# Performance work log

Measured on AMD Instinct MI355X. Metric: run time of the kernel, lower is better.

Reference implementation:

```python
import jax, jax.numpy as jnp
import numpy as np

NUM_HEADS = 16
EPS = 1e-6

def _rmsnorm(h, w):
    h32 = h.astype(jnp.float32)
    var = jnp.mean(h32 * h32, axis=-1, keepdims=True)
    return (w * (h32 * jax.lax.rsqrt(var + EPS))).astype(h.dtype)

def setup_inputs() -> dict:
    key = jax.random.key(0)
    ks = jax.random.split(key, 4)
    B, N, C = 16, 1024, 1024
    x = jax.random.normal(ks[0], (B, N, C), dtype=jnp.float32)
    qkv_w = jax.random.normal(ks[1], (3 * C, C), dtype=jnp.float32) * (C ** -0.5)
    proj_w = jax.random.normal(ks[2], (C, C), dtype=jnp.float32) * (C ** -0.5)
    proj_b = jnp.zeros((C,), dtype=jnp.float32)
    q_norm_w = jnp.ones((C // NUM_HEADS,), dtype=jnp.float32)
    k_norm_w = jnp.ones((C // NUM_HEADS,), dtype=jnp.float32)
    return {"x": x, "qkv_w": qkv_w, "proj_w": proj_w, "proj_b": proj_b,
            "q_norm_w": q_norm_w, "k_norm_w": k_norm_w}

def reference(x, qkv_w, proj_w, proj_b, q_norm_w, k_norm_w):
    B, N, C = x.shape
    H = NUM_HEADS
    Dh = C // H
    scale = Dh ** -0.5  # qk_scale default; temperature = 1.0
    # QKV projection (no bias): [B,N,3,H,Dh]
    qkv = (x @ qkv_w.T).reshape(B, N, 3, H, Dh)
    q, k, v = qkv[:, :, 0], qkv[:, :, 1], qkv[:, :, 2]
    # per-head QK RMSNorm (fp32 internally)
    q = _rmsnorm(q, q_norm_w)
    k = _rmsnorm(k, k_norm_w)
    # explicit softmax attention: [B,H,N,N]
    attn = jnp.einsum('bnhd,bmhd->bhnm', q * scale, k)
    attn = jax.nn.softmax(attn, axis=-1)
    out = jnp.einsum('bhnm,bmhd->bnhd', attn, v).reshape(B, N, C)
    return out @ proj_w.T + proj_b
```

## Files before the change

### kernel.cpp

```cpp
#include <hip/hip_runtime.h>
#include <hip/hip_bf16.h>

typedef __attribute__((ext_vector_type(8))) __bf16 bf16x8;
typedef __attribute__((ext_vector_type(4))) __bf16 bf16x4;
typedef __attribute__((ext_vector_type(4))) float f32x4;

#define AS1(p) ((__attribute__((address_space(1))) void*)(p))
#define AS3(p) ((__attribute__((address_space(3))) void*)(p))

__global__ void f2b_kernel(const float4* __restrict__ in, bf16x4* __restrict__ out, int n4) {
    int idx = blockIdx.x * blockDim.x + threadIdx.x;
    int stride = gridDim.x * blockDim.x;
    for (int i = idx; i < n4; i += stride) {
        float4 v = in[i];
        bf16x4 o;
        o[0] = (__bf16)v.x; o[1] = (__bf16)v.y; o[2] = (__bf16)v.z; o[3] = (__bf16)v.w;
        out[i] = o;
    }
}

template<int MODE>
__global__ __launch_bounds__(512, 2)
void gemm256(const __bf16* __restrict__ A, const __bf16* __restrict__ Bw,
             const float* __restrict__ bias, const float* __restrict__ qw,
             const float* __restrict__ kw, float* __restrict__ Cf,
             __bf16* __restrict__ Cb, __bf16* __restrict__ Vt,
             int M, int K, int nbn, int ldc)
{
    __shared__ __bf16 Asl[4][256 * 32];
    __shared__ __bf16 Bsl[4][256 * 32];
    const int tid = threadIdx.x, l = tid & 63, w = tid >> 6;
    const int fr = l & 15, fk = l >> 4;

    const int cpx = gridDim.x >> 3;
    const int wg = (blockIdx.x & 7) * cpx + (blockIdx.x >> 3);
    const int bm = wg / nbn, bn = wg % nbn;

    const __bf16* Ag = A + (size_t)bm * 256 * K;
    const __bf16* Bg = Bw + (size_t)bn * 256 * K;

    const int arow = tid >> 2;
    const int uch = (tid & 3) ^ ((arow >> 1) & 3);
    const size_t ga = (size_t)arow * K + uch * 8;
    const size_t ga2 = ga + (size_t)128 * K;

    const int axc = (fk ^ ((fr >> 1) & 3)) * 16;
    int aoff[8], boff[4];
    #pragma unroll
    for (int m = 0; m < 8; ++m)
        aoff[m] = ((w >> 2) * 128 + m * 16 + fr) * 64 + axc;
    #pragma unroll
    for (int n = 0; n < 4; ++n)
        boff[n] = ((w & 3) * 64 + n * 16 + fr) * 64 + axc;

    f32x4 acc[8][4] = {};

#define STAGE256(S) do {                                                                    \
    const int sb_ = (S) & 3;                                                                \
    __builtin_amdgcn_global_load_lds(AS1(Ag + (size_t)(S) * 32 + ga),                       \
        AS3((char*)&Asl[sb_][0] + tid * 16), 16, 0, 0);                                     \
    __builtin_amdgcn_global_load_lds(AS1(Ag + (size_t)(S) * 32 + ga2),                      \
        AS3((char*)&Asl[sb_][0] + tid * 16 + 8192), 16, 0, 0);                              \
    __builtin_amdgcn_global_load_lds(AS1(Bg + (size_t)(S) * 32 + ga),                       \
        AS3((char*)&Bsl[sb_][0] + tid * 16), 16, 0, 0);                                     \
    __builtin_amdgcn_global_load_lds(AS1(Bg + (size_t)(S) * 32 + ga2),                      \
        AS3((char*)&Bsl[sb_][0] + tid * 16 + 8192), 16, 0, 0);                              \
} while (0)

#define PHASE256(S, VMSTR, DOSTAGE) do {                                                    \
    asm volatile("s_waitcnt vmcnt(" VMSTR ")" ::: "memory");                                \
    __builtin_amdgcn_s_barrier();                                                           \
    __builtin_amdgcn_sched_barrier(0);                                                      \
    const int pb_ = (S) & 3;                                                                \
    bf16x8 af[8], bfv[4];                                                                   \
    _Pragma("unroll")                                                                       \
    for (int m = 0; m < 8; ++m)                                                             \
        af[m] = *(const bf16x8*)((const char*)&Asl[pb_][0] + aoff[m]);                      \
    _Pragma("unroll")                                                                       \
    for (int n = 0; n < 4; ++n)                                                             \
        bfv[n] = *(const bf16x8*)((const char*)&Bsl[pb_][0] + boff[n]);                     \
    if (DOSTAGE) STAGE256((S) + 3);                                                         \
    __builtin_amdgcn_s_setprio(1);                                                          \
    _Pragma("unroll")                                                                       \
    for (int m = 0; m < 8; ++m)                                                             \
        _Pragma("unroll")                                                                   \
        for (int n = 0; n < 4; ++n)                                                         \
            acc[m][n] = __builtin_amdgcn_mfma_f32_16x16x32_bf16(af[m], bfv[n], acc[m][n], 0, 0, 0); \
    __builtin_amdgcn_s_setprio(0);                                                          \
} while (0)

    const int S = K >> 5;
    STAGE256(0); STAGE256(1); STAGE256(2);
    for (int s = 0; s < S - 2; ++s)
        PHASE256(s, "8", (s + 3 < S));
    PHASE256(S - 2, "4", false);
    PHASE256(S - 1, "0", false);
#undef PHASE256
#undef STAGE256

    const int rb0 = bm * 256 + (w >> 2) * 128 + fk * 4;
    const int cb0 = bn * 256 + (w & 3) * 64;

    if (MODE == 1) {
        #pragma unroll
        for (int m = 0; m < 8; ++m)
            #pragma unroll
            for (int n = 0; n < 4; ++n) {
                const int col = cb0 + n * 16 + fr;
                const float bv = bias[col];
                #pragma unroll
                for (int r = 0; r < 4; ++r)
                    Cf[(size_t)(rb0 + m * 16 + r) * ldc + col] = acc[m][n][r] + bv;
            }
    } else {
        const int sect = bn >> 2;
        if (sect < 2) {
            const float* wp = (sect == 0) ? qw : kw;
            float wn[4];
            #pragma unroll
            for (int n = 0; n < 4; ++n) wn[n] = wp[((w & 3) * 64 + n * 16 + fr) & 63];
            #pragma unroll
            for (int m = 0; m < 8; ++m) {
                float sc[4];
                #pragma unroll
                for (int r = 0; r < 4; ++r) {
                    float ps = 0.f;
                    #pragma unroll
                    for (int n = 0; n < 4; ++n) ps += acc[m][n][r] * acc[m][n][r];
                    ps += __shfl_xor(ps, 1); ps += __shfl_xor(ps, 2);
                    ps += __shfl_xor(ps, 4); ps += __shfl_xor(ps, 8);
                    sc[r] = rsqrtf(ps * (1.0f / 64.0f) + 1e-6f);
                    if (sect == 0) sc[r] *= 0.18033688011112042f;
                }
                #pragma unroll
                for (int n = 0; n < 4; ++n)
                    #pragma unroll
                    for (int r = 0; r < 4; ++r)
                        Cb[(size_t)(rb0 + m * 16 + r) * ldc + cb0 + n * 16 + fr] =
                            (__bf16)(acc[m][n][r] * sc[r] * wn[n]);
            }
        } else {
            #pragma unroll
            for (int m = 0; m < 8; ++m) {
                const int tok = rb0 + m * 16;
                const int b = tok >> 10, ntok = tok & 1023;
                #pragma unroll
                for (int n = 0; n < 4; ++n) {
                    const int vd = (bn - 8) * 256 + (w & 3) * 64 + n * 16 + fr;
                    bf16x4 pk;
                    #pragma unroll
                    for (int r = 0; r < 4; ++r) pk[r] = (__bf16)acc[m][n][r];
                    *(bf16x4*)&Vt[((size_t)((b * 16 + (vd >> 6)) * 64 + (vd & 63))) * 1024 + ntok] = pk;
                }
            }
        }
    }
}

__global__ __launch_bounds__(256, 2)
void attn_kernel(const __bf16* __restrict__ qkv, const __bf16* __restrict__ vt,
                 __bf16* __restrict__ ao)
{
    __shared__ __bf16 Ks[4][64 * 64];
    __shared__ __bf16 Vs[4][64 * 64];
    __shared__ __bf16 Pl[4][2 * 16 * 64];
    const int tid = threadIdx.x, l = tid & 63, w = tid >> 6;
    const int fr = l & 15, fk = l >> 4;
    const int sw = (fr & 7) << 4;

    const int bi = blockIdx.x;
    const int L = (bi & 7) * 128 + (bi >> 3);
    const int qb = L & 3, h = (L >> 2) & 15, b = L >> 6;

    const __bf16* Kg = qkv + (size_t)b * 1024 * 2048 + 1024 + h * 64;
    const __bf16* Vg = vt + (size_t)((b * 16 + h) * 64) * 1024;
    const int srow = tid >> 3, scp = tid & 7;

    const int c8 = (scp ^ (srow & 7)) * 8;
    const size_t kO0 = (size_t)srow * 2048 + c8, kO1 = kO0 + 32 * 2048;
    const size_t vO0 = (size_t)srow * 1024 + c8, vO1 = vO0 + 32 * 1024;
    char* ksd = (char*)&Ks[0][0] + tid * 16;
    char* vsd = (char*)&Vs[0][0] + tid * 16;

#define STAGE(KT) do {                                                                    \
    char* dk_ = ksd + ((KT) & 3) * 8192;                                                  \
    char* dv_ = vsd + ((KT) & 3) * 8192;                                                  \
    __builtin_amdgcn_global_load_lds(AS1(Kg + (size_t)(KT) * 131072 + kO0), AS3(dk_), 16, 0, 0); \
    __builtin_amdgcn_global_load_lds(AS1(Kg + (size_t)(KT) * 131072 + kO1), AS3(dk_ + 4096), 16, 0, 0); \
    __builtin_amdgcn_global_load_lds(AS1(Vg + (KT) * 64 + vO0), AS3(dv_), 16, 0, 0);      \
    __builtin_amdgcn_global_load_lds(AS1(Vg + (KT) * 64 + vO1), AS3(dv_ + 4096), 16, 0, 0); \
} while (0)

    STAGE(0); STAGE(1);

    const int qrow0 = b * 1024 + qb * 256 + w * 64;
    bf16x8 qf[4][2];
    #pragma unroll
    for (int qi = 0; qi < 4; ++qi)
        #pragma unroll
        for (int dc = 0; dc < 2; ++dc)
            qf[qi][dc] = *(const bf16x8*)&qkv[(size_t)(qrow0 + qi * 16 + fr) * 2048
                                              + h * 64 + dc * 32 + fk * 8];

    const int kb0 = fr * 128 + ((fk ^ (fr & 7)) * 16);
    const int kb1 = fr * 128 + (((4 + fk) ^ (fr & 7)) * 16);
    const char* KsB = (const char*)&Ks[0][0];
    const char* VsB = (const char*)&Vs[0][0];

    char* Pw = (char*)&Pl[w][0];
    const int pw0 = (fr * 128 + 0 * 32 + fk * 8) ^ sw;
    const int pw1 = (fr * 128 + 1 * 32 + fk * 8) ^ sw;
    const int pw2 = (fr * 128 + 2 * 32 + fk * 8) ^ sw;
    const int pw3 = (fr * 128 + 3 * 32 + fk * 8) ^ sw;
    const int pr0 = (fr * 128 + 0 * 64 + fk * 16) ^ sw;
    const int pr1 = (fr * 128 + 1 * 64 + fk * 16) ^ sw;

    bf16x8 onesf;
    #pragma unroll
    for (int i = 0; i < 8; ++i) onesf[i] = (__bf16)1.0f;

    f32x4 oacc[4][4] = {};
    f32x4 lacc[4] = {};

    for (int p = 0; p < 8; ++p) {
        asm volatile("s_waitcnt vmcnt(0)" ::: "memory");
        __builtin_amdgcn_s_barrier();
        __builtin_amdgcn_sched_barrier(0);
        if (p < 7) { STAGE(2 * p + 2); STAGE(2 * p + 3); }

        #pragma unroll
        for (int kh = 0; kh < 2; ++kh) {
            const int cb = (((p & 1) << 1) | kh) * 8192;
            bf16x8 kf[4][2], vf[4][2];
            #pragma unroll
            for (int n = 0; n < 4; ++n) {
                kf[n][0] = *(const bf16x8*)(KsB + cb + kb0 + n * 2048);
                kf[n][1] = *(const bf16x8*)(KsB + cb + kb1 + n * 2048);
            }
            #pragma unroll
            for (int nd = 0; nd < 4; ++nd) {
                vf[nd][0] = *(const bf16x8*)(VsB + cb + kb0 + nd * 2048);
                vf[nd][1] = *(const bf16x8*)(VsB + cb + kb1 + nd * 2048);
            }

            #pragma unroll
            for (int qi = 0; qi < 4; ++qi) {
                const int pq = (qi & 1) * 2048;
                f32x4 sacc[4] = {};
                #pragma unroll
                for (int n = 0; n < 4; ++n)
                    #pragma unroll
                    for (int dc = 0; dc < 2; ++dc)
                        sacc[n] = __builtin_amdgcn_mfma_f32_16x16x32_bf16(kf[n][dc], qf[qi][dc],
                                                                          sacc[n], 0, 0, 0);

                #pragma unroll
                for (int n = 0; n < 4; ++n) {
                    bf16x4 pk;
                    #pragma unroll
                    for (int r = 0; r < 4; ++r)
                        pk[r] = (__bf16)__builtin_amdgcn_exp2f(sacc[n][r]);
                    const int pwn = (n == 0) ? pw0 : (n == 1) ? pw1 : (n == 2) ? pw2 : pw3;
                    *(bf16x4*)(Pw + pq + pwn) = pk;
                }

                bf16x8 pf0 = *(const bf16x8*)(Pw + pq + pr0);
                bf16x8 pf1 = *(const bf16x8*)(Pw + pq + pr1);
                lacc[qi] = __builtin_amdgcn_mfma_f32_16x16x32_bf16(pf0, onesf, lacc[qi], 0, 0, 0);
                lacc[qi] = __builtin_amdgcn_mfma_f32_16x16x32_bf16(pf1, onesf, lacc[qi], 0, 0, 0);
                #pragma unroll
                for (int nd = 0; nd < 4; ++nd) {
                    oacc[qi][nd] = __builtin_amdgcn_mfma_f32_16x16x32_bf16(pf0, vf[nd][0],
                                                                           oacc[qi][nd], 0, 0, 0);
                    oacc[qi][nd] = __builtin_amdgcn_mfma_f32_16x16x32_bf16(pf1, vf[nd][1],
                                                                           oacc[qi][nd], 0, 0, 0);
                }
            }
        }
    }

    #pragma unroll
    for (int qi = 0; qi < 4; ++qi) {
        float inv[4];
        #pragma unroll
        for (int r = 0; r < 4; ++r)
            inv[r] = __builtin_amdgcn_rcpf(lacc[qi][r]);
        #pragma unroll
        for (int nd = 0; nd < 4; ++nd)
            #pragma unroll
            for (int r = 0; r < 4; ++r)
                ao[(size_t)(qrow0 + qi * 16 + fk * 4 + r) * 1024 + h * 64 + nd * 16 + fr] =
                    (__bf16)(oacc[qi][nd][r] * inv[r]);
    }
#undef STAGE
}

extern "C" void kernel_launch(void* const* d_in, const int* in_sizes, int n_in,
                              void* d_out, int out_size, void* d_ws, size_t ws_size,
                              hipStream_t stream)
{
    const float* x      = (const float*)d_in[0];
    const float* qkv_w  = (const float*)d_in[1];
    const float* proj_w = (const float*)d_in[2];
    const float* proj_b = (const float*)d_in[3];
    const float* qnw    = (const float*)d_in[4];
    const float* knw    = (const float*)d_in[5];

    char* ws = (char*)d_ws;
    __bf16* xb    = (__bf16*)(ws);
    __bf16* wqkv  = (__bf16*)(ws + 33554432);
    __bf16* wproj = (__bf16*)(ws + 39845888);
    __bf16* qkv   = (__bf16*)(ws + 41943040);
    __bf16* vt    = (__bf16*)(ws + 109051904);
    __bf16* ao    = (__bf16*)(ws + 142606336);

    f2b_kernel<<<2048, 256, 0, stream>>>((const float4*)x,      (bf16x4*)xb,    16777216 / 4);
    f2b_kernel<<<2048, 256, 0, stream>>>((const float4*)qkv_w,  (bf16x4*)wqkv,  3145728 / 4);
    f2b_kernel<<<1024, 256, 0, stream>>>((const float4*)proj_w, (bf16x4*)wproj, 1048576 / 4);

    gemm256<0><<<768, 512, 0, stream>>>(xb, wqkv, nullptr, qnw, knw,
                                        nullptr, qkv, vt, 16384, 1024, 12, 2048);
    attn_kernel<<<1024, 256, 0, stream>>>(qkv, vt, ao);
    gemm256<1><<<256, 512, 0, stream>>>(ao, wproj, proj_b, nullptr, nullptr,
                                        (float*)d_out, nullptr, nullptr, 16384, 1024, 4, 1024);
}
```

Before: 255.6 us.

## Software-pipeline QK and PV MFMAs in attention; merge weight cast kernels

The attention inner loop is restructured so the QK^T MFMAs and exp for the next query tile are issued while the PV and row-sum MFMAs for the current tile run, using the double-buffered per-wave P scratch. K fragments are now loaded inside the QK step and V fragments are reloaded at the half-point. This hides the latency of exp and the LDS round-trip for P behind matrix work, at the cost of more live registers. Separately, the two weight fp32-to-bf16 casts are merged into one launch to save a kernel launch.

```diff
diff --git a/kernel.cpp b/kernel.cpp
--- a/kernel.cpp
+++ b/kernel.cpp
@@ -16,6 +16,18 @@
         bf16x4 o;
         o[0] = (__bf16)v.x; o[1] = (__bf16)v.y; o[2] = (__bf16)v.z; o[3] = (__bf16)v.w;
         out[i] = o;
+    }
+}
+
+__global__ void f2b2_kernel(const float4* __restrict__ a, bf16x4* __restrict__ oa, int na4,
+                            const float4* __restrict__ b, bf16x4* __restrict__ ob, int nb4) {
+    int idx = blockIdx.x * blockDim.x + threadIdx.x;
+    int stride = gridDim.x * blockDim.x;
+    for (int i = idx; i < na4 + nb4; i += stride) {
+        const float4 v = (i < na4) ? a[i] : b[i - na4];
+        bf16x4 o;
+        o[0] = (__bf16)v.x; o[1] = (__bf16)v.y; o[2] = (__bf16)v.z; o[3] = (__bf16)v.w;
+        if (i < na4) oa[i] = o; else ob[i - na4] = o;
     }
 }
 
@@ -222,60 +234,80 @@
     f32x4 oacc[4][4] = {};
     f32x4 lacc[4] = {};
 
+#define QK8(SA, QI, CB) do {                                                              \
+    _Pragma("unroll")                                                                     \
+    for (int n_ = 0; n_ < 4; ++n_) {                                                      \
+        bf16x8 k0_ = *(const bf16x8*)(KsB + (CB) + kb0 + n_ * 2048);                      \
+        bf16x8 k1_ = *(const bf16x8*)(KsB + (CB) + kb1 + n_ * 2048);                      \
+        SA[n_] = __builtin_amdgcn_mfma_f32_16x16x32_bf16(k0_, qf[QI][0], SA[n_], 0, 0, 0);\
+        SA[n_] = __builtin_amdgcn_mfma_f32_16x16x32_bf16(k1_, qf[QI][1], SA[n_], 0, 0, 0);\
+    } } while (0)
+
+#define EXPW(SA, PQ) do {                                                                 \
+    _Pragma("unroll")                                                                     \
+    for (int n_ = 0; n_ < 4; ++n_) {                                                      \
+        bf16x4 pk_;                                                                       \
+        _Pragma("unroll")                                                                 \
+        for (int r_ = 0; r_ < 4; ++r_)                                                    \
+            pk_[r_] = (__bf16)__builtin_amdgcn_exp2f(SA[n_][r_]);                         \
+        const int pwn_ = (n_ == 0) ? pw0 : (n_ == 1) ? pw1 : (n_ == 2) ? pw2 : pw3;       \
+        *(bf16x4*)(Pw + (PQ) + pwn_) = pk_;                                               \
+    } } while (0)
+
     for (int p = 0; p < 8; ++p) {
         asm volatile("s_waitcnt vmcnt(0)" ::: "memory");
         __builtin_amdgcn_s_barrier();
         __builtin_amdgcn_sched_barrier(0);
         if (p < 7) { STAGE(2 * p + 2); STAGE(2 * p + 3); }
 
-        #pragma unroll
-        for (int kh = 0; kh < 2; ++kh) {
-            const int cb = (((p & 1) << 1) | kh) * 8192;
-            bf16x8 kf[4][2], vf[4][2];
-            #pragma unroll
-            for (int n = 0; n < 4; ++n) {
-                kf[n][0] = *(const bf16x8*)(KsB + cb + kb0 + n * 2048);
-                kf[n][1] = *(const bf16x8*)(KsB + cb + kb1 + n * 2048);
-            }
+        const int cb0 = ((p & 1) << 1) * 8192;
+        const int cb1 = cb0 + 8192;
+
+        bf16x8 vf[4][2];
+        #pragma unroll
+        for (int nd = 0; nd < 4; ++nd) {
+            vf[nd][0] = *(const bf16x8*)(VsB + cb0 + kb0 + nd * 2048);
+            vf[nd][1] = *(const bf16x8*)(VsB + cb0 + kb1 + nd * 2048);
+        }
+
+        {
+            f32x4 s0[4] = {};
+            QK8(s0, 0, cb0);
+            EXPW(s0, 0);
+        }
+
+        #pragma unroll
+        for (int j = 0; j < 8; ++j) {
+            const int qi = j & 3;
+            const int pq = (j & 1) * 2048;
+            const int pqn = ((j + 1) & 1) * 2048;
+            const int cbn = (j + 1 < 4) ? cb0 : cb1;
+
+            bf16x8 pf0 = *(const bf16x8*)(Pw + pq + pr0);
+            bf16x8 pf1 = *(const bf16x8*)(Pw + pq + pr1);
+
+            if (j == 4) {
+                #pragma unroll
+                for (int nd = 0; nd < 4; ++nd) {
+                    vf[nd][0] = *(const bf16x8*)(VsB + cb1 + kb0 + nd * 2048);
+                    vf[nd][1] = *(const bf16x8*)(VsB + cb1 + kb1 + nd * 2048);
+                }
+            }
+
+            f32x4 sn[4] = {};
+            if (j < 7) QK8(sn, (j + 1) & 3, cbn);
+
+            lacc[qi] = __builtin_amdgcn_mfma_f32_16x16x32_bf16(pf0, onesf, lacc[qi], 0, 0, 0);
+            lacc[qi] = __builtin_amdgcn_mfma_f32_16x16x32_bf16(pf1, onesf, lacc[qi], 0, 0, 0);
             #pragma unroll
             for (int nd = 0; nd < 4; ++nd) {
-                vf[nd][0] = *(const bf16x8*)(VsB + cb + kb0 + nd * 2048);
-                vf[nd][1] = *(const bf16x8*)(VsB + cb + kb1 + nd * 2048);
-            }
-
-            #pragma unroll
-            for (int qi = 0; qi < 4; ++qi) {
-                const int pq = (qi & 1) * 2048;
-                f32x4 sacc[4] = {};
-                #pragma unroll
-                for (int n = 0; n < 4; ++n)
-                    #pragma unroll
-                    for (int dc = 0; dc < 2; ++dc)
-                        sacc[n] = __builtin_amdgcn_mfma_f32_16x16x32_bf16(kf[n][dc], qf[qi][dc],
-                                                                          sacc[n], 0, 0, 0);
-
-                #pragma unroll
-                for (int n = 0; n < 4; ++n) {
-                    bf16x4 pk;
-                    #pragma unroll
-                    for (int r = 0; r < 4; ++r)
-                        pk[r] = (__bf16)__builtin_amdgcn_exp2f(sacc[n][r]);
-                    const int pwn = (n == 0) ? pw0 : (n == 1) ? pw1 : (n == 2) ? pw2 : pw3;
-                    *(bf16x4*)(Pw + pq + pwn) = pk;
-                }
-
-                bf16x8 pf0 = *(const bf16x8*)(Pw + pq + pr0);
-                bf16x8 pf1 = *(const bf16x8*)(Pw + pq + pr1);
-                lacc[qi] = __builtin_amdgcn_mfma_f32_16x16x32_bf16(pf0, onesf, lacc[qi], 0, 0, 0);
-                lacc[qi] = __builtin_amdgcn_mfma_f32_16x16x32_bf16(pf1, onesf, lacc[qi], 0, 0, 0);
-                #pragma unroll
-                for (int nd = 0; nd < 4; ++nd) {
-                    oacc[qi][nd] = __builtin_amdgcn_mfma_f32_16x16x32_bf16(pf0, vf[nd][0],
-                                                                           oacc[qi][nd], 0, 0, 0);
-                    oacc[qi][nd] = __builtin_amdgcn_mfma_f32_16x16x32_bf16(pf1, vf[nd][1],
-                                                                           oacc[qi][nd], 0, 0, 0);
-                }
-            }
+                oacc[qi][nd] = __builtin_amdgcn_mfma_f32_16x16x32_bf16(pf0, vf[nd][0],
+                                                                       oacc[qi][nd], 0, 0, 0);
+                oacc[qi][nd] = __builtin_amdgcn_mfma_f32_16x16x32_bf16(pf1, vf[nd][1],
+                                                                       oacc[qi][nd], 0, 0, 0);
+            }
+
+            if (j < 7) EXPW(sn, pqn);
         }
     }
 
@@ -292,6 +324,8 @@
                 ao[(size_t)(qrow0 + qi * 16 + fk * 4 + r) * 1024 + h * 64 + nd * 16 + fr] =
                     (__bf16)(oacc[qi][nd][r] * inv[r]);
     }
+#undef QK8
+#undef EXPW
 #undef STAGE
 }
 
@@ -314,9 +348,9 @@
     __bf16* vt    = (__bf16*)(ws + 109051904);
     __bf16* ao    = (__bf16*)(ws + 142606336);
 
-    f2b_kernel<<<2048, 256, 0, stream>>>((const float4*)x,      (bf16x4*)xb,    16777216 / 4);
-    f2b_kernel<<<2048, 256, 0, stream>>>((const float4*)qkv_w,  (bf16x4*)wqkv,  3145728 / 4);
-    f2b_kernel<<<1024, 256, 0, stream>>>((const float4*)proj_w, (bf16x4*)wproj, 1048576 / 4);
+    f2b_kernel<<<2048, 256, 0, stream>>>((const float4*)x, (bf16x4*)xb, 16777216 / 4);
+    f2b2_kernel<<<2048, 256, 0, stream>>>((const float4*)qkv_w,  (bf16x4*)wqkv,  3145728 / 4,
+                                          (const float4*)proj_w, (bf16x4*)wproj, 1048576 / 4);
 
     gemm256<0><<<768, 512, 0, stream>>>(xb, wqkv, nullptr, qnw, knw,
                                         nullptr, qkv, vt, 16384, 1024, 12, 2048);
```

Measured after the change: 253.2 us, median of 5. About the same (-0.9%).
